# Optimization experiments

Hardware: AMD Instinct MI355X
Metric: run time of the kernel (lower is better)

The kernel has to match this reference:

```python
import jax, jax.numpy as jnp
import numpy as np

B, D, L = 512, 512, 24

def setup_inputs() -> dict:
    key = jax.random.key(0)
    k1, k2 = jax.random.split(key)
    source = jax.random.normal(k1, (B, D), dtype=jnp.float32)
    s_labels = jax.random.randint(k2, (B, L), 0, 2, dtype=jnp.int32)
    return {"source": source, "s_labels": s_labels}

def reference(source, s_labels):
    margin = 0.0
    squared = False
    # pairwise squared euclidean distances, (B, B)
    diff = source[:, None, :] - source[None, :, :]          # (B, B, D)
    dist = jnp.clip(jnp.sum(diff * diff, axis=-1), 0.0)     # (B, B)
    if not squared:
        zmask = (dist == 0.0).astype(dist.dtype)
        dist = jnp.sqrt(dist + zmask * 1e-16) * (1.0 - zmask)
    # triplet validity mask: labels[i]==labels[j] (share a label) and labels[i]!=labels[k]
    lab = s_labels.astype(jnp.float32)
    sim = (lab @ lab.T > 0).astype(jnp.float32)              # (B, B)
    mask = sim[:, :, None] * (1.0 - sim[:, None, :])         # (B, B, B)
    # euclidean branch: d_ap - (1 - margin) * d_an
    triplet = dist[:, :, None] - (1.0 - margin) * dist[:, None, :]
    triplet = jnp.clip(mask * triplet, 0.0)                  # (B, B, B)
    num_positive = jnp.sum((triplet > 1e-16).astype(jnp.float32))
    return jnp.sum(triplet) / (num_positive + 1e-16)
```

## Files before the change

### kernel.cpp

```cpp
#include <hip/hip_runtime.h>

#define BN 512
#define DD 512
#define LL 24


__global__ void prep_kernel(const float* __restrict__ src, const int* __restrict__ labels,
                            float* __restrict__ norms, unsigned* __restrict__ masks,
                            float* __restrict__ accum) {
    int i = blockIdx.x;
    int lane = threadIdx.x;
    const float4* row = (const float4*)(src + (size_t)i * DD);
    float4 v0 = row[lane];
    float4 v1 = row[lane + 64];
    float s = v0.x*v0.x + v0.y*v0.y + v0.z*v0.z + v0.w*v0.w
            + v1.x*v1.x + v1.y*v1.y + v1.z*v1.z + v1.w*v1.w;
#pragma unroll
    for (int off = 32; off > 0; off >>= 1) s += __shfl_down(s, off);
    int lab = (lane < LL) ? labels[i * LL + lane] : 0;
    unsigned long long b = __ballot(lab != 0);
    if (lane == 0) {
        norms[i] = s;
        masks[i] = (unsigned)(b & 0xFFFFFFull);
        if (i == 0) { accum[0] = 0.0f; ((unsigned*)accum)[1] = 0u; }
    }
}

__device__ __forceinline__ float dist_val(float d2, bool diag) {
    d2 = fmaxf(d2, 0.0f);
    float d = sqrtf(d2);
    return diag ? 0.0f : d;
}

__global__ void dist_kernel(const float* __restrict__ S, const float* __restrict__ norms,
                            float* __restrict__ Dm) {
    __shared__ float As[32][34];
    __shared__ float Bs[32][34];
    int t  = threadIdx.x;
    int tx = t & 15, ty = t >> 4;
    int jb = blockIdx.x * 32;
    int ib = blockIdx.y * 32;
    int lr = t >> 3;
    int lc = (t & 7) * 4;
    float acc00 = 0.f, acc01 = 0.f, acc10 = 0.f, acc11 = 0.f;
    for (int k0 = 0; k0 < DD; k0 += 32) {
        float4 a = *(const float4*)&S[(size_t)(ib + lr) * DD + k0 + lc];
        float4 b = *(const float4*)&S[(size_t)(jb + lr) * DD + k0 + lc];
        As[lc + 0][lr] = a.x; As[lc + 1][lr] = a.y; As[lc + 2][lr] = a.z; As[lc + 3][lr] = a.w;
        Bs[lc + 0][lr] = b.x; Bs[lc + 1][lr] = b.y; Bs[lc + 2][lr] = b.z; Bs[lc + 3][lr] = b.w;
        __syncthreads();
#pragma unroll
        for (int kk = 0; kk < 32; kk++) {
            float2 av = *(const float2*)&As[kk][ty * 2];
            float2 bv = *(const float2*)&Bs[kk][tx * 2];
            acc00 += av.x * bv.x; acc01 += av.x * bv.y;
            acc10 += av.y * bv.x; acc11 += av.y * bv.y;
        }
        __syncthreads();
    }
    int i0 = ib + ty * 2, j0 = jb + tx * 2;
    float ni0 = norms[i0], ni1 = norms[i0 + 1];
    float nj0 = norms[j0], nj1 = norms[j0 + 1];
    float2 r0, r1;
    r0.x = dist_val(ni0 + nj0 - 2.f * acc00, i0     == j0    );
    r0.y = dist_val(ni0 + nj1 - 2.f * acc01, i0     == j0 + 1);
    r1.x = dist_val(ni1 + nj0 - 2.f * acc10, i0 + 1 == j0    );
    r1.y = dist_val(ni1 + nj1 - 2.f * acc11, i0 + 1 == j0 + 1);
    *(float2*)&Dm[(size_t)i0 * BN + j0]     = r0;
    *(float2*)&Dm[(size_t)(i0+1) * BN + j0] = r1;
}

__global__ void triplet_kernel(const float* __restrict__ Dm, const unsigned* __restrict__ masks,
                               float* __restrict__ accum) {
    __shared__ float pos[BN];
    __shared__ float neg[BN];
    __shared__ int pcnt, ncnt;
    __shared__ float wsum[4];
    __shared__ unsigned wcnt[4];
    const int i = blockIdx.x;
    const int t = threadIdx.x;
    const int lane = t & 63;
    const int w = t >> 6;
    if (t == 0) { pcnt = 0; ncnt = 0; }
    __syncthreads();
    const unsigned mi = masks[i];
    const float* drow = Dm + (size_t)i * BN;
    const unsigned long long ltmask = (1ull << lane) - 1ull;

    for (int j = t; j < BN; j += 256) {
        float dj = drow[j];
        bool isp = (mi & masks[j]) != 0u;
        unsigned long long bal = __ballot(isp);
        int np = __popcll(bal);
        if (np > 0) {
            int ldr = __ffsll((unsigned long long)bal) - 1;
            int base = 0;
            if (lane == ldr) base = atomicAdd(&pcnt, np);
            base = __shfl(base, ldr);
            if (isp) pos[base + __popcll(bal & ltmask)] = dj;
        }
        unsigned long long nbal = ~bal;
        int nn = 64 - np;
        if (nn > 0) {
            int ldr = __ffsll((unsigned long long)nbal) - 1;
            int base = 0;
            if (lane == ldr) base = atomicAdd(&ncnt, nn);
            base = __shfl(base, ldr);
            if (!isp) neg[base + __popcll(nbal & ltmask)] = dj;
        }
    }
    __syncthreads();

    const int P = pcnt, N = ncnt;
    float sum = 0.f;
    unsigned cnt = 0;
    for (int p = t; p < P; p += 256) {
        float a = pos[p];
        for (int n = 0; n < N; n++) {
            float v = a - neg[n];
            sum += fmaxf(v, 0.0f);
            cnt += (v > 1e-16f) ? 1u : 0u;
        }
    }
#pragma unroll
    for (int off = 32; off > 0; off >>= 1) {
        sum += __shfl_down(sum, off);
        cnt += __shfl_down(cnt, off);
    }
    if (lane == 0) { wsum[w] = sum; wcnt[w] = cnt; }
    __syncthreads();
    if (t == 0) {
        sum = wsum[0] + wsum[1] + wsum[2] + wsum[3];
        cnt = wcnt[0] + wcnt[1] + wcnt[2] + wcnt[3];
        if (sum != 0.f || cnt != 0u) {
            atomicAdd(&accum[0], sum);
            atomicAdd(&((unsigned*)accum)[1], cnt);
        }
    }
}

__global__ void finalize_kernel(const float* __restrict__ accum, float* __restrict__ out) {
    if (threadIdx.x == 0) {
        float s = accum[0];
        float c = (float)((const unsigned*)accum)[1];
        out[0] = s / (c + 1e-16f);
    }
}

extern "C" void kernel_launch(void* const* d_in, const int* in_sizes, int n_in,
                              void* d_out, int out_size, void* d_ws, size_t ws_size,
                              hipStream_t stream) {
    const float* src    = (const float*)d_in[0];
    const int*   labels = (const int*)d_in[1];
    float* ws = (float*)d_ws;
    float*    norms = ws;
    unsigned* masks = (unsigned*)(ws + BN);
    float*    Dm    = ws + 2 * BN;
    float*    accum = ws + 2 * BN + (size_t)BN * BN;

    hipLaunchKernelGGL(prep_kernel,     dim3(BN),     dim3(64),  0, stream, src, labels, norms, masks, accum);
    hipLaunchKernelGGL(dist_kernel,     dim3(16, 16), dim3(256), 0, stream, src, norms, Dm);
    hipLaunchKernelGGL(triplet_kernel,  dim3(BN),     dim3(256), 0, stream, Dm, masks, accum);
    hipLaunchKernelGGL(finalize_kernel, dim3(1),      dim3(64),  0, stream, accum, (float*)d_out);
}
```

Measured before the change: 78.71 us.

## Compute pairwise distance Gram matrix with split-bf16 MFMA instead of FP32 FMA

The prep kernel now splits each source value into a bf16 high part and a bf16 residual and stores both arrays. The distance kernel replaces the shared-memory FP32 tiled GEMM with a single-wavefront-per-tile kernel using 16x16x32 bf16 MFMA. It does three products (hi*hi, hi*lo, lo*hi) with register prefetch of the next K slice. This targets the vector-ALU cost of the Gram matrix, at the price of extra workspace traffic and a small precision loss from dropping the lo*lo term.

```diff
diff --git a/kernel.cpp b/kernel.cpp
--- a/kernel.cpp
+++ b/kernel.cpp
@@ -4,9 +4,22 @@
 #define DD 512
 #define LL 24
 
+typedef unsigned short u16;
+typedef __attribute__((ext_vector_type(8))) short short8;
+typedef __attribute__((ext_vector_type(4))) float f32x4;
+
+
+__device__ __forceinline__ u16 bf16_rn(float f) {
+    unsigned u = __float_as_uint(f);
+    return (u16)((u + 0x7FFFu + ((u >> 16) & 1u)) >> 16);
+}
+__device__ __forceinline__ float bf16_f(u16 h) {
+    return __uint_as_float(((unsigned)h) << 16);
+}
 
 __global__ void prep_kernel(const float* __restrict__ src, const int* __restrict__ labels,
                             float* __restrict__ norms, unsigned* __restrict__ masks,
+                            u16* __restrict__ Sh, u16* __restrict__ Sl,
                             float* __restrict__ accum) {
     int i = blockIdx.x;
     int lane = threadIdx.x;
@@ -15,6 +28,27 @@
     float4 v1 = row[lane + 64];
     float s = v0.x*v0.x + v0.y*v0.y + v0.z*v0.z + v0.w*v0.w
             + v1.x*v1.x + v1.y*v1.y + v1.z*v1.z + v1.w*v1.w;
+
+    float f[8] = {v0.x, v0.y, v0.z, v0.w, v1.x, v1.y, v1.z, v1.w};
+    u16 hi[8], lo[8];
+#pragma unroll
+    for (int e = 0; e < 8; e++) {
+        hi[e] = bf16_rn(f[e]);
+        lo[e] = bf16_rn(f[e] - bf16_f(hi[e]));
+    }
+    size_t o0 = (size_t)i * DD + 4 * lane;
+    size_t o1 = o0 + 256;
+    uint2 h0 = make_uint2((unsigned)hi[0] | ((unsigned)hi[1] << 16),
+                          (unsigned)hi[2] | ((unsigned)hi[3] << 16));
+    uint2 h1 = make_uint2((unsigned)hi[4] | ((unsigned)hi[5] << 16),
+                          (unsigned)hi[6] | ((unsigned)hi[7] << 16));
+    uint2 l0 = make_uint2((unsigned)lo[0] | ((unsigned)lo[1] << 16),
+                          (unsigned)lo[2] | ((unsigned)lo[3] << 16));
+    uint2 l1 = make_uint2((unsigned)lo[4] | ((unsigned)lo[5] << 16),
+                          (unsigned)lo[6] | ((unsigned)lo[7] << 16));
+    *(uint2*)(Sh + o0) = h0;  *(uint2*)(Sh + o1) = h1;
+    *(uint2*)(Sl + o0) = l0;  *(uint2*)(Sl + o1) = l1;
+
 #pragma unroll
     for (int off = 32; off > 0; off >>= 1) s += __shfl_down(s, off);
     int lab = (lane < LL) ? labels[i * LL + lane] : 0;
@@ -32,42 +66,70 @@
     return diag ? 0.0f : d;
 }
 
-__global__ void dist_kernel(const float* __restrict__ S, const float* __restrict__ norms,
-                            float* __restrict__ Dm) {
-    __shared__ float As[32][34];
-    __shared__ float Bs[32][34];
-    int t  = threadIdx.x;
-    int tx = t & 15, ty = t >> 4;
-    int jb = blockIdx.x * 32;
-    int ib = blockIdx.y * 32;
-    int lr = t >> 3;
-    int lc = (t & 7) * 4;
-    float acc00 = 0.f, acc01 = 0.f, acc10 = 0.f, acc11 = 0.f;
+__global__ __launch_bounds__(64) void dist_mfma_kernel(
+    const u16* __restrict__ Sh, const u16* __restrict__ Sl,
+    const float* __restrict__ norms, float* __restrict__ Dm)
+{
+    const int l    = threadIdx.x;
+    const int r    = l & 15;
+    const int half = l >> 4;
+    const int jb = blockIdx.x * 32;
+    const int ib = blockIdx.y * 32;
+    const int kb = half * 8;
+
+    const u16* pA0h = Sh + (size_t)(ib + r)      * DD + kb;
+    const u16* pA1h = Sh + (size_t)(ib + 16 + r) * DD + kb;
+    const u16* pB0h = Sh + (size_t)(jb + r)      * DD + kb;
+    const u16* pB1h = Sh + (size_t)(jb + 16 + r) * DD + kb;
+    const u16* pA0l = Sl + (size_t)(ib + r)      * DD + kb;
+    const u16* pA1l = Sl + (size_t)(ib + 16 + r) * DD + kb;
+    const u16* pB0l = Sl + (size_t)(jb + r)      * DD + kb;
+    const u16* pB1l = Sl + (size_t)(jb + 16 + r) * DD + kb;
+
+    f32x4 acc00 = {0.f,0.f,0.f,0.f}, acc01 = acc00, acc10 = acc00, acc11 = acc00;
+
+    short8 a0h = *(const short8*)(pA0h), a1h = *(const short8*)(pA1h);
+    short8 b0h = *(const short8*)(pB0h), b1h = *(const short8*)(pB1h);
+    short8 a0l = *(const short8*)(pA0l), a1l = *(const short8*)(pA1l);
+    short8 b0l = *(const short8*)(pB0l), b1l = *(const short8*)(pB1l);
+
     for (int k0 = 0; k0 < DD; k0 += 32) {
-        float4 a = *(const float4*)&S[(size_t)(ib + lr) * DD + k0 + lc];
-        float4 b = *(const float4*)&S[(size_t)(jb + lr) * DD + k0 + lc];
-        As[lc + 0][lr] = a.x; As[lc + 1][lr] = a.y; As[lc + 2][lr] = a.z; As[lc + 3][lr] = a.w;
-        Bs[lc + 0][lr] = b.x; Bs[lc + 1][lr] = b.y; Bs[lc + 2][lr] = b.z; Bs[lc + 3][lr] = b.w;
-        __syncthreads();
-#pragma unroll
-        for (int kk = 0; kk < 32; kk++) {
-            float2 av = *(const float2*)&As[kk][ty * 2];
-            float2 bv = *(const float2*)&Bs[kk][tx * 2];
-            acc00 += av.x * bv.x; acc01 += av.x * bv.y;
-            acc10 += av.y * bv.x; acc11 += av.y * bv.y;
-        }
-        __syncthreads();
-    }
-    int i0 = ib + ty * 2, j0 = jb + tx * 2;
-    float ni0 = norms[i0], ni1 = norms[i0 + 1];
-    float nj0 = norms[j0], nj1 = norms[j0 + 1];
-    float2 r0, r1;
-    r0.x = dist_val(ni0 + nj0 - 2.f * acc00, i0     == j0    );
-    r0.y = dist_val(ni0 + nj1 - 2.f * acc01, i0     == j0 + 1);
-    r1.x = dist_val(ni1 + nj0 - 2.f * acc10, i0 + 1 == j0    );
-    r1.y = dist_val(ni1 + nj1 - 2.f * acc11, i0 + 1 == j0 + 1);
-    *(float2*)&Dm[(size_t)i0 * BN + j0]     = r0;
-    *(float2*)&Dm[(size_t)(i0+1) * BN + j0] = r1;
+        short8 na0h, na1h, nb0h, nb1h, na0l, na1l, nb0l, nb1l;
+        const int kn = k0 + 32;
+        if (kn < DD) {
+            na0h = *(const short8*)(pA0h + kn); na1h = *(const short8*)(pA1h + kn);
+            nb0h = *(const short8*)(pB0h + kn); nb1h = *(const short8*)(pB1h + kn);
+            na0l = *(const short8*)(pA0l + kn); na1l = *(const short8*)(pA1l + kn);
+            nb0l = *(const short8*)(pB0l + kn); nb1l = *(const short8*)(pB1l + kn);
+        }
+        acc00 = __builtin_amdgcn_mfma_f32_16x16x32_bf16(a0h, b0h, acc00, 0, 0, 0);
+        acc01 = __builtin_amdgcn_mfma_f32_16x16x32_bf16(a0h, b1h, acc01, 0, 0, 0);
+        acc10 = __builtin_amdgcn_mfma_f32_16x16x32_bf16(a1h, b0h, acc10, 0, 0, 0);
+        acc11 = __builtin_amdgcn_mfma_f32_16x16x32_bf16(a1h, b1h, acc11, 0, 0, 0);
+        acc00 = __builtin_amdgcn_mfma_f32_16x16x32_bf16(a0h, b0l, acc00, 0, 0, 0);
+        acc01 = __builtin_amdgcn_mfma_f32_16x16x32_bf16(a0h, b1l, acc01, 0, 0, 0);
+        acc10 = __builtin_amdgcn_mfma_f32_16x16x32_bf16(a1h, b0l, acc10, 0, 0, 0);
+        acc11 = __builtin_amdgcn_mfma_f32_16x16x32_bf16(a1h, b1l, acc11, 0, 0, 0);
+        acc00 = __builtin_amdgcn_mfma_f32_16x16x32_bf16(a0l, b0h, acc00, 0, 0, 0);
+        acc01 = __builtin_amdgcn_mfma_f32_16x16x32_bf16(a0l, b1h, acc01, 0, 0, 0);
+        acc10 = __builtin_amdgcn_mfma_f32_16x16x32_bf16(a1l, b0h, acc10, 0, 0, 0);
+        acc11 = __builtin_amdgcn_mfma_f32_16x16x32_bf16(a1l, b1h, acc11, 0, 0, 0);
+        a0h = na0h; a1h = na1h; b0h = nb0h; b1h = nb1h;
+        a0l = na0l; a1l = na1l; b0l = nb0l; b1l = nb1l;
+    }
+
+    const int jc0 = jb + r, jc1 = jb + 16 + r;
+    const float nj0 = norms[jc0], nj1 = norms[jc1];
+#pragma unroll
+    for (int p = 0; p < 4; p++) {
+        const int ir0 = ib + half * 4 + p;
+        const int ir1 = ir0 + 16;
+        const float ni0 = norms[ir0], ni1 = norms[ir1];
+        Dm[(size_t)ir0 * BN + jc0] = dist_val(ni0 + nj0 - 2.f * acc00[p], ir0 == jc0);
+        Dm[(size_t)ir0 * BN + jc1] = dist_val(ni0 + nj1 - 2.f * acc01[p], ir0 == jc1);
+        Dm[(size_t)ir1 * BN + jc0] = dist_val(ni1 + nj0 - 2.f * acc10[p], ir1 == jc0);
+        Dm[(size_t)ir1 * BN + jc1] = dist_val(ni1 + nj1 - 2.f * acc11[p], ir1 == jc1);
+    }
 }
 
 __global__ void triplet_kernel(const float* __restrict__ Dm, const unsigned* __restrict__ masks,
@@ -156,10 +218,16 @@
     float*    norms = ws;
     unsigned* masks = (unsigned*)(ws + BN);
     float*    Dm    = ws + 2 * BN;
-    float*    accum = ws + 2 * BN + (size_t)BN * BN;
-
-    hipLaunchKernelGGL(prep_kernel,     dim3(BN),     dim3(64),  0, stream, src, labels, norms, masks, accum);
-    hipLaunchKernelGGL(dist_kernel,     dim3(16, 16), dim3(256), 0, stream, src, norms, Dm);
-    hipLaunchKernelGGL(triplet_kernel,  dim3(BN),     dim3(256), 0, stream, Dm, masks, accum);
-    hipLaunchKernelGGL(finalize_kernel, dim3(1),      dim3(64),  0, stream, accum, (float*)d_out);
-}
+    u16*      Sh    = (u16*)(ws + 2 * BN + (size_t)BN * BN);
+    u16*      Sl    = Sh + (size_t)BN * DD;
+    float*    accum = ws + 2 * BN + (size_t)BN * BN + BN * DD;
+
+    hipLaunchKernelGGL(prep_kernel,      dim3(BN),     dim3(64),  0, stream,
+                       src, labels, norms, masks, Sh, Sl, accum);
+    hipLaunchKernelGGL(dist_mfma_kernel, dim3(16, 16), dim3(64),  0, stream,
+                       Sh, Sl, norms, Dm);
+    hipLaunchKernelGGL(triplet_kernel,   dim3(BN),     dim3(256), 0, stream,
+                       Dm, masks, accum);
+    hipLaunchKernelGGL(finalize_kernel,  dim3(1),      dim3(64),  0, stream,
+                       accum, (float*)d_out);
+}
```

Measured after the change: 75.10 us. 1.05x faster.
